# Kernel tuning notes

Measured on AMD Instinct MI355X. Metric: run time of the kernel, lower is better.

## Reference

```python
import jax, jax.numpy as jnp
import numpy as np

N_NODES = 200000
N_EDGES = 1000000
N_GRAPHS = 4096
F_IN = 11
H = 64


def setup_inputs() -> dict:
    key = jax.random.key(0)
    ks = jax.random.split(key, 8)
    x = jax.random.normal(ks[0], (N_NODES, F_IN), jnp.float32)
    edge_index = jax.random.randint(ks[1], (2, N_EDGES), 0, N_NODES, jnp.int32)
    batch = jnp.sort(jax.random.randint(ks[2], (N_NODES,), 0, N_GRAPHS, jnp.int32))
    def glorot(k, shape):
        fan_in, fan_out = shape[0], shape[1]
        s = jnp.sqrt(6.0 / (fan_in + fan_out))
        return jax.random.uniform(k, shape, jnp.float32, -s, s)
    return {
        "x": x,
        "edge_index": edge_index,
        "batch": batch,
        "W1": glorot(ks[3], (F_IN, H)),
        "b1": jnp.zeros((H,), jnp.float32),
        "W2": glorot(ks[4], (H, H)),
        "b2": jnp.zeros((H,), jnp.float32),
        "W3": glorot(ks[5], (H, H)),
        "b3": jnp.zeros((H,), jnp.float32),
        "lin_w": glorot(ks[6], (H, 1)),
        "lin_b": jnp.zeros((1,), jnp.float32),
    }


def _gcn_conv(x, W, b, src, dst, norm, num_nodes):
    # linear transform then gather-scale-scatter (PyG GCNConv, source_to_target)
    h = x @ W                                   # [N, out]
    msg = h[src] * norm[:, None]                # [E+N, out]
    out = jax.ops.segment_sum(msg, dst, num_segments=num_nodes)
    return out + b


def reference(x, edge_index, batch, W1, b1, W2, b2, W3, b3, lin_w, lin_b):
    n = x.shape[0]
    # add self-loops (gcn_norm with add_self_loops=True)
    loops = jnp.arange(n, dtype=edge_index.dtype)
    src = jnp.concatenate([edge_index[0], loops])
    dst = jnp.concatenate([edge_index[1], loops])
    deg = jax.ops.segment_sum(jnp.ones_like(dst, x.dtype), dst, num_segments=n)
    dis = jnp.where(deg > 0, jax.lax.rsqrt(jnp.maximum(deg, 1.0)), 0.0)
    norm = dis[src] * dis[dst]                  # symmetric normalization

    h = jax.nn.relu(_gcn_conv(x, W1, b1, src, dst, norm, n))
    h = jax.nn.relu(_gcn_conv(h, W2, b2, src, dst, norm, n))
    h = _gcn_conv(h, W3, b3, src, dst, norm, n)  # no relu after conv3

    # global mean pool over graph ids
    sums = jax.ops.segment_sum(h, batch, num_segments=N_GRAPHS)
    cnts = jax.ops.segment_sum(jnp.ones((n,), h.dtype), batch, num_segments=N_GRAPHS)
    pooled = sums / jnp.maximum(cnts, 1.0)[:, None]
    # dropout is identity in eval mode
    return pooled @ lin_w + lin_b
```

## Files before the change

kernel.cpp:

```cpp
#include <hip/hip_runtime.h>
#include <hip/hip_fp16.h>

#define N_NODES 200000
#define N_EDGES 1000000
#define N_GRAPHS 4096
#define F_IN 11
#define H 64
#define XP 16
#define CAP 32


__global__ void place_direct_kernel(const int* __restrict__ src, const int* __restrict__ dst,
                                    int* __restrict__ cnt, int* __restrict__ csr) {
    int e = blockIdx.x * blockDim.x + threadIdx.x;
    if (e < N_EDGES) {
        int d = dst[e];
        int p = atomicAdd(&cnt[d], 1);
        if (p < CAP) csr[(size_t)d * CAP + p] = src[e];
    }
}

__global__ void dis_cnt_kernel(const int* __restrict__ cnt, const int* __restrict__ batch,
                               float* __restrict__ dis, int* __restrict__ gcnt) {
    int i = blockIdx.x * blockDim.x + threadIdx.x;
    if (i < N_NODES) {
        dis[i] = rsqrtf((float)(cnt[i] + 1));
        atomicAdd(&gcnt[batch[i]], 1);
    }
}


__global__ void w3l_kernel(const float* __restrict__ W3, const float* __restrict__ lw,
                           float* __restrict__ w3l) {
    int k = threadIdx.x;
    if (k < H) {
        float s = 0.f;
#pragma unroll
        for (int j = 0; j < H; ++j) s += W3[k * H + j] * lw[j];
        w3l[k] = s;
    }
}


__global__ void xscale_kernel(const float* __restrict__ x, const float* __restrict__ dis,
                              __half* __restrict__ xsh) {
    int i = blockIdx.x * blockDim.x + threadIdx.x;
    if (i < N_NODES * XP) {
        int row = i >> 4;
        int c = i & 15;
        float v = (c < F_IN) ? x[(size_t)row * F_IN + c] * dis[row] : 0.f;
        xsh[i] = __float2half_rn(v);
    }
}


__global__ void gather1_kernel(const int* __restrict__ cnt, const int* __restrict__ csr,
                               const __half* __restrict__ xsh, const float* __restrict__ dis,
                               __half* __restrict__ P) {
    int lane = threadIdx.x & 63;
    int j = lane & 3;
    int g = lane >> 2;
    int wave = (blockIdx.x * blockDim.x + threadIdx.x) >> 6;
    int nw = (gridDim.x * blockDim.x) >> 6;
    for (int n = wave; n < N_NODES; n += nw) {
        int deg = cnt[n]; if (deg > CAP) deg = CAP;
        int nslots = deg + 1;
        const int* crow = csr + (size_t)n * CAP;
        __half2 hacc0 = __float2half2_rn(0.f);
        __half2 hacc1 = __float2half2_rn(0.f);
        for (int base = 0; base < nslots; base += 16) {
            int slot = base + g;
            if (slot < nslots) {
                int s = (slot == 0) ? n : crow[slot - 1];
                union { uint2 u; __half2 h[2]; } r;
                r.u = *(const uint2*)(xsh + (size_t)s * XP + j * 4);
                hacc0 = __hadd2(hacc0, r.h[0]);
                hacc1 = __hadd2(hacc1, r.h[1]);
            }
        }
        float2 f0 = __half22float2(hacc0);
        float2 f1 = __half22float2(hacc1);
        float a0 = f0.x, a1 = f0.y, a2 = f1.x, a3 = f1.y;
#pragma unroll
        for (int m = 4; m <= 32; m <<= 1) {
            a0 += __shfl_xor(a0, m, 64);
            a1 += __shfl_xor(a1, m, 64);
            a2 += __shfl_xor(a2, m, 64);
            a3 += __shfl_xor(a3, m, 64);
        }
        if (g == 0) {
            float d = dis[n];
            union { uint2 u; __half2 h[2]; } pk;
            pk.h[0] = __floats2half2_rn(a0 * d, a1 * d);
            pk.h[1] = __floats2half2_rn(a2 * d, a3 * d);
            *(uint2*)(P + (size_t)n * XP + j * 4) = pk.u;
        }
    }
}


__global__ void gemm_fused_kernel(const __half* __restrict__ Ph,
                                  const float* __restrict__ W1, const float* __restrict__ b1,
                                  const float* __restrict__ W2, const float* __restrict__ dis,
                                  __half* __restrict__ Bsh) {
    __shared__ float Xt[XP][68];
    __shared__ float W1s[F_IN][64];
    __shared__ float H1t[64][68];
    __shared__ float W2s[64][64];
    int tid = threadIdx.x;
    int rowbase = blockIdx.x * 64;

    for (int i = tid; i < F_IN * 64; i += 256) W1s[i >> 6][i & 63] = W1[i];
    for (int i = tid; i < 64 * 64; i += 256) W2s[i >> 6][i & 63] = W2[i];
    {
        int r = tid >> 2;
        int c4 = (tid & 3) * 4;
        union { uint2 u; __half2 h[2]; } v;
        v.u = *(const uint2*)(Ph + (size_t)(rowbase + r) * XP + c4);
        float2 f0 = __half22float2(v.h[0]);
        float2 f1 = __half22float2(v.h[1]);
        Xt[c4 + 0][r] = f0.x;
        Xt[c4 + 1][r] = f0.y;
        Xt[c4 + 2][r] = f1.x;
        Xt[c4 + 3][r] = f1.y;
    }
    __syncthreads();

    int tc = (tid & 15) * 4;
    int tr = (tid >> 4) * 4;

    {
        float a[4][4] = {{0}};
#pragma unroll
        for (int k = 0; k < F_IN; ++k) {
            float4 xv = *(const float4*)&Xt[k][tr];
            float4 wv = *(const float4*)&W1s[k][tc];
            float xs4[4] = {xv.x, xv.y, xv.z, xv.w};
            float ws4[4] = {wv.x, wv.y, wv.z, wv.w};
#pragma unroll
            for (int i = 0; i < 4; ++i)
#pragma unroll
                for (int j = 0; j < 4; ++j) a[i][j] += xs4[i] * ws4[j];
        }
        float4 bv = *(const float4*)(b1 + tc);
        float bj[4] = {bv.x, bv.y, bv.z, bv.w};
#pragma unroll
        for (int i = 0; i < 4; ++i)
#pragma unroll
            for (int j = 0; j < 4; ++j)
                H1t[tc + j][tr + i] = fmaxf(a[i][j] + bj[j], 0.f);
    }
    __syncthreads();

    float c00 = 0, c01 = 0, c02 = 0, c03 = 0;
    float c10 = 0, c11 = 0, c12 = 0, c13 = 0;
    float c20 = 0, c21 = 0, c22 = 0, c23 = 0;
    float c30 = 0, c31 = 0, c32 = 0, c33 = 0;
#pragma unroll
    for (int k = 0; k < 64; ++k) {
        float4 xv = *(const float4*)&H1t[k][tr];
        float4 wv = *(const float4*)&W2s[k][tc];
        c00 += xv.x * wv.x; c01 += xv.x * wv.y; c02 += xv.x * wv.z; c03 += xv.x * wv.w;
        c10 += xv.y * wv.x; c11 += xv.y * wv.y; c12 += xv.y * wv.z; c13 += xv.y * wv.w;
        c20 += xv.z * wv.x; c21 += xv.z * wv.y; c22 += xv.z * wv.z; c23 += xv.z * wv.w;
        c30 += xv.w * wv.x; c31 += xv.w * wv.y; c32 += xv.w * wv.z; c33 += xv.w * wv.w;
    }
    float cc[4][4] = {{c00, c01, c02, c03}, {c10, c11, c12, c13},
                      {c20, c21, c22, c23}, {c30, c31, c32, c33}};
#pragma unroll
    for (int i = 0; i < 4; ++i) {
        int row = rowbase + tr + i;
        float d = dis[row];
        union { uint2 u; __half2 h[2]; } pk;
        pk.h[0] = __floats2half2_rn(cc[i][0] * d, cc[i][1] * d);
        pk.h[1] = __floats2half2_rn(cc[i][2] * d, cc[i][3] * d);
        *(uint2*)(Bsh + (size_t)row * 64 + tc) = pk.u;
    }
}


__global__ void gather_fused_kernel(const int* __restrict__ cnt,
                                    const int* __restrict__ csr,
                                    const __half* __restrict__ Bsh,
                                    const float* __restrict__ dis,
                                    const float* __restrict__ b2,
                                    const float* __restrict__ w3l,
                                    float* __restrict__ y) {
    int lane = threadIdx.x & 63;
    int j = lane & 7;
    int g = lane >> 3;
    int wave = (blockIdx.x * blockDim.x + threadIdx.x) >> 6;
    int nw = (gridDim.x * blockDim.x) >> 6;
    float4 bi0 = *(const float4*)(b2 + j * 8);
    float4 bi1 = *(const float4*)(b2 + j * 8 + 4);
    float4 wl0 = *(const float4*)(w3l + j * 8);
    float4 wl1 = *(const float4*)(w3l + j * 8 + 4);
    for (int n = wave; n < N_NODES; n += nw) {
        int deg = cnt[n]; if (deg > CAP) deg = CAP;
        int nslots = deg + 1;
        const int* crow = csr + (size_t)n * CAP;
        __half2 hacc[4];
#pragma unroll
        for (int k = 0; k < 4; ++k) hacc[k] = __float2half2_rn(0.f);
        for (int base = 0; base < nslots; base += 8) {
            int slot = base + g;
            if (slot < nslots) {
                int s = (slot == 0) ? n : crow[slot - 1];
                union { uint4 u; __half2 h[4]; } r;
                r.u = *(const uint4*)(Bsh + (size_t)s * 64 + j * 8);
#pragma unroll
                for (int k = 0; k < 4; ++k) hacc[k] = __hadd2(hacc[k], r.h[k]);
            }
        }
        float acc[8];
#pragma unroll
        for (int k = 0; k < 4; ++k) {
            float2 f = __half22float2(hacc[k]);
            acc[2 * k] = f.x; acc[2 * k + 1] = f.y;
        }
#pragma unroll
        for (int m = 8; m <= 32; m <<= 1) {
#pragma unroll
            for (int k = 0; k < 8; ++k) acc[k] += __shfl_xor(acc[k], m, 64);
        }
        if (g == 0) {
            float d = dis[n];
            float bi[8] = {bi0.x, bi0.y, bi0.z, bi0.w, bi1.x, bi1.y, bi1.z, bi1.w};
            float wl[8] = {wl0.x, wl0.y, wl0.z, wl0.w, wl1.x, wl1.y, wl1.z, wl1.w};
            float p = 0.f;
#pragma unroll
            for (int k = 0; k < 8; ++k)
                p += fmaxf(acc[k] * d + bi[k], 0.f) * wl[k];
            p += __shfl_xor(p, 1, 64);
            p += __shfl_xor(p, 2, 64);
            p += __shfl_xor(p, 4, 64);
            if (j == 0) y[n] = p * d;
        }
    }
}


__global__ void pool_scalar_kernel(const int* __restrict__ cnt,
                                   const int* __restrict__ csr,
                                   const float* __restrict__ y,
                                   const float* __restrict__ dis,
                                   const int* __restrict__ batch,
                                   float* __restrict__ gsum) {
    int lane = threadIdx.x & 63;
    int u = lane >> 4;
    int t = lane & 15;
    int wave = (blockIdx.x * blockDim.x + threadIdx.x) >> 6;
    int n = wave * 4 + u;
    int deg = cnt[n]; if (deg > CAP) deg = CAP;
    int nslots = deg + 1;
    const int* crow = csr + (size_t)n * CAP;
    float acc = 0.f;
    for (int base = 0; base < nslots; base += 16) {
        int slot = base + t;
        if (slot < nslots) {
            int s = (slot == 0) ? n : crow[slot - 1];
            acc += y[s];
        }
    }
    acc += __shfl_xor(acc, 1, 64);
    acc += __shfl_xor(acc, 2, 64);
    acc += __shfl_xor(acc, 4, 64);
    acc += __shfl_xor(acc, 8, 64);
    if (t == 0) atomicAdd(&gsum[batch[n]], acc * dis[n]);
}


__global__ void head2_kernel(const float* __restrict__ gsum, const int* __restrict__ gcnt,
                             const float* __restrict__ b3, const float* __restrict__ lw,
                             const float* __restrict__ lb, float* __restrict__ out) {
    int g = blockIdx.x * blockDim.x + threadIdx.x;
    if (g >= N_GRAPHS) return;
    float cb = 0.f;
#pragma unroll
    for (int k = 0; k < H; ++k) cb += b3[k] * lw[k];
    int c = gcnt[g];
    out[g] = (c > 0) ? (gsum[g] / (float)c + cb + lb[0]) : lb[0];
}

extern "C" void kernel_launch(void* const* d_in, const int* in_sizes, int n_in,
                              void* d_out, int out_size, void* d_ws, size_t ws_size,
                              hipStream_t stream) {
    const float* x     = (const float*)d_in[0];
    const int*   ei    = (const int*)d_in[1];
    const int*   batch = (const int*)d_in[2];
    const float* W1    = (const float*)d_in[3];
    const float* b1    = (const float*)d_in[4];
    const float* W2    = (const float*)d_in[5];
    const float* b2    = (const float*)d_in[6];
    const float* W3    = (const float*)d_in[7];
    const float* b3    = (const float*)d_in[8];
    const float* lw    = (const float*)d_in[9];
    const float* lb    = (const float*)d_in[10];
    float* out = (float*)d_out;

    const int* src = ei;
    const int* dst = ei + N_EDGES;

    char* ws = (char*)d_ws;
    const size_t MB = 1u << 20;
    int*    cnt  = (int*)ws;
    float*  y    = (float*)(ws + 1 * MB);
    float*  dis  = (float*)(ws + 2 * MB);
    int*    csr  = (int*)(ws + 4 * MB);
    __half* xsh  = (__half*)(ws + 30 * MB);
    __half* Ph   = (__half*)(ws + 37 * MB);
    __half* Bsh  = (__half*)(ws + 44 * MB);
    float*  gsum = (float*)(ws + 70 * MB);
    int*    gcnt = (int*)(ws + 70 * MB + 16384);
    float*  w3l  = (float*)(ws + 70 * MB + 32768);

    const int BT = 256;
    const int gemm_grid = N_NODES / 64;
    const int gath_grid = 2048;

    hipMemsetAsync(cnt, 0, (size_t)N_NODES * 4, stream);
    hipMemsetAsync(gsum, 0, (size_t)N_GRAPHS * 8, stream);
    place_direct_kernel<<<(N_EDGES + BT - 1) / BT, BT, 0, stream>>>(src, dst, cnt, csr);
    dis_cnt_kernel<<<(N_NODES + BT - 1) / BT, BT, 0, stream>>>(cnt, batch, dis, gcnt);
    w3l_kernel<<<1, 64, 0, stream>>>(W3, lw, w3l);

    xscale_kernel<<<(N_NODES * XP + BT - 1) / BT, BT, 0, stream>>>(x, dis, xsh);
    gather1_kernel<<<gath_grid, BT, 0, stream>>>(cnt, csr, xsh, dis, Ph);
    gemm_fused_kernel<<<gemm_grid, BT, 0, stream>>>(Ph, W1, b1, W2, dis, Bsh);

    gather_fused_kernel<<<gath_grid, BT, 0, stream>>>(cnt, csr, Bsh, dis, b2, w3l, y);

    pool_scalar_kernel<<<N_NODES / 16, BT, 0, stream>>>(cnt, csr, y, dis, batch, gsum);

    head2_kernel<<<(N_GRAPHS + BT - 1) / BT, BT, 0, stream>>>(gsum, gcnt, b3, lw, lb, out);
}
```

Baseline: 394.2 us.

## Fuse degree normalization into xscale, process two nodes per wave in gathers

Removes the separate dis_cnt kernel by computing rsqrt degree and the per-graph node counts inside xscale_kernel. Both gather kernels now handle two nodes per wave iteration, interleaving their neighbor loads for more memory-level parallelism at the cost of extra registers and divergence when degrees differ. The pooling kernel uses 8 lanes per node instead of 16, covering more nodes per wave. Each lane recomputes rsqrt from cnt, which adds redundant loads.

```diff
diff --git a/kernel.cpp b/kernel.cpp
--- a/kernel.cpp
+++ b/kernel.cpp
@@ -20,15 +20,6 @@
     }
 }
 
-__global__ void dis_cnt_kernel(const int* __restrict__ cnt, const int* __restrict__ batch,
-                               float* __restrict__ dis, int* __restrict__ gcnt) {
-    int i = blockIdx.x * blockDim.x + threadIdx.x;
-    if (i < N_NODES) {
-        dis[i] = rsqrtf((float)(cnt[i] + 1));
-        atomicAdd(&gcnt[batch[i]], 1);
-    }
-}
-
 
 __global__ void w3l_kernel(const float* __restrict__ W3, const float* __restrict__ lw,
                            float* __restrict__ w3l) {
@@ -42,13 +33,19 @@
 }
 
 
-__global__ void xscale_kernel(const float* __restrict__ x, const float* __restrict__ dis,
-                              __half* __restrict__ xsh) {
+__global__ void xscale_kernel(const float* __restrict__ x, const int* __restrict__ cnt,
+                              const int* __restrict__ batch, float* __restrict__ dis,
+                              int* __restrict__ gcnt, __half* __restrict__ xsh) {
     int i = blockIdx.x * blockDim.x + threadIdx.x;
     if (i < N_NODES * XP) {
         int row = i >> 4;
         int c = i & 15;
-        float v = (c < F_IN) ? x[(size_t)row * F_IN + c] * dis[row] : 0.f;
+        float d = rsqrtf((float)(cnt[row] + 1));
+        if (c == 0) {
+            dis[row] = d;
+            atomicAdd(&gcnt[batch[row]], 1);
+        }
+        float v = (c < F_IN) ? x[(size_t)row * F_IN + c] * d : 0.f;
         xsh[i] = __float2half_rn(v);
     }
 }
@@ -62,38 +59,54 @@
     int g = lane >> 2;
     int wave = (blockIdx.x * blockDim.x + threadIdx.x) >> 6;
     int nw = (gridDim.x * blockDim.x) >> 6;
-    for (int n = wave; n < N_NODES; n += nw) {
-        int deg = cnt[n]; if (deg > CAP) deg = CAP;
-        int nslots = deg + 1;
-        const int* crow = csr + (size_t)n * CAP;
-        __half2 hacc0 = __float2half2_rn(0.f);
-        __half2 hacc1 = __float2half2_rn(0.f);
-        for (int base = 0; base < nslots; base += 16) {
+    for (int n0 = wave * 2; n0 < N_NODES; n0 += nw * 2) {
+        int n1 = n0 + 1;
+        int d0 = cnt[n0]; if (d0 > CAP) d0 = CAP;
+        int d1 = cnt[n1]; if (d1 > CAP) d1 = CAP;
+        int ns0 = d0 + 1, ns1 = d1 + 1;
+        const int* crow0 = csr + (size_t)n0 * CAP;
+        const int* crow1 = csr + (size_t)n1 * CAP;
+        __half2 a0h0 = __float2half2_rn(0.f), a0h1 = a0h0;
+        __half2 a1h0 = a0h0, a1h1 = a0h0;
+        int maxns = ns0 > ns1 ? ns0 : ns1;
+        for (int base = 0; base < maxns; base += 16) {
             int slot = base + g;
-            if (slot < nslots) {
-                int s = (slot == 0) ? n : crow[slot - 1];
+            if (slot < ns0) {
+                int s = (slot == 0) ? n0 : crow0[slot - 1];
                 union { uint2 u; __half2 h[2]; } r;
                 r.u = *(const uint2*)(xsh + (size_t)s * XP + j * 4);
-                hacc0 = __hadd2(hacc0, r.h[0]);
-                hacc1 = __hadd2(hacc1, r.h[1]);
-            }
-        }
-        float2 f0 = __half22float2(hacc0);
-        float2 f1 = __half22float2(hacc1);
-        float a0 = f0.x, a1 = f0.y, a2 = f1.x, a3 = f1.y;
+                a0h0 = __hadd2(a0h0, r.h[0]);
+                a0h1 = __hadd2(a0h1, r.h[1]);
+            }
+            if (slot < ns1) {
+                int s = (slot == 0) ? n1 : crow1[slot - 1];
+                union { uint2 u; __half2 h[2]; } r;
+                r.u = *(const uint2*)(xsh + (size_t)s * XP + j * 4);
+                a1h0 = __hadd2(a1h0, r.h[0]);
+                a1h1 = __hadd2(a1h1, r.h[1]);
+            }
+        }
+        float2 f00 = __half22float2(a0h0), f01 = __half22float2(a0h1);
+        float2 f10 = __half22float2(a1h0), f11 = __half22float2(a1h1);
+        float v0[4] = {f00.x, f00.y, f01.x, f01.y};
+        float v1[4] = {f10.x, f10.y, f11.x, f11.y};
 #pragma unroll
         for (int m = 4; m <= 32; m <<= 1) {
-            a0 += __shfl_xor(a0, m, 64);
-            a1 += __shfl_xor(a1, m, 64);
-            a2 += __shfl_xor(a2, m, 64);
-            a3 += __shfl_xor(a3, m, 64);
+#pragma unroll
+            for (int k = 0; k < 4; ++k) {
+                v0[k] += __shfl_xor(v0[k], m, 64);
+                v1[k] += __shfl_xor(v1[k], m, 64);
+            }
         }
         if (g == 0) {
-            float d = dis[n];
+            float dd0 = dis[n0], dd1 = dis[n1];
             union { uint2 u; __half2 h[2]; } pk;
-            pk.h[0] = __floats2half2_rn(a0 * d, a1 * d);
-            pk.h[1] = __floats2half2_rn(a2 * d, a3 * d);
-            *(uint2*)(P + (size_t)n * XP + j * 4) = pk.u;
+            pk.h[0] = __floats2half2_rn(v0[0] * dd0, v0[1] * dd0);
+            pk.h[1] = __floats2half2_rn(v0[2] * dd0, v0[3] * dd0);
+            *(uint2*)(P + (size_t)n0 * XP + j * 4) = pk.u;
+            pk.h[0] = __floats2half2_rn(v1[0] * dd1, v1[1] * dd1);
+            pk.h[1] = __floats2half2_rn(v1[2] * dd1, v1[3] * dd1);
+            *(uint2*)(P + (size_t)n1 * XP + j * 4) = pk.u;
         }
     }
 }
@@ -195,46 +208,69 @@
     float4 bi1 = *(const float4*)(b2 + j * 8 + 4);
     float4 wl0 = *(const float4*)(w3l + j * 8);
     float4 wl1 = *(const float4*)(w3l + j * 8 + 4);
-    for (int n = wave; n < N_NODES; n += nw) {
-        int deg = cnt[n]; if (deg > CAP) deg = CAP;
-        int nslots = deg + 1;
-        const int* crow = csr + (size_t)n * CAP;
-        __half2 hacc[4];
-#pragma unroll
-        for (int k = 0; k < 4; ++k) hacc[k] = __float2half2_rn(0.f);
-        for (int base = 0; base < nslots; base += 8) {
+    for (int n0 = wave * 2; n0 < N_NODES; n0 += nw * 2) {
+        int n1 = n0 + 1;
+        int d0 = cnt[n0]; if (d0 > CAP) d0 = CAP;
+        int d1 = cnt[n1]; if (d1 > CAP) d1 = CAP;
+        int ns0 = d0 + 1, ns1 = d1 + 1;
+        const int* crow0 = csr + (size_t)n0 * CAP;
+        const int* crow1 = csr + (size_t)n1 * CAP;
+        __half2 ha[4], hb[4];
+#pragma unroll
+        for (int k = 0; k < 4; ++k) { ha[k] = __float2half2_rn(0.f); hb[k] = ha[k]; }
+        int maxns = ns0 > ns1 ? ns0 : ns1;
+        for (int base = 0; base < maxns; base += 8) {
             int slot = base + g;
-            if (slot < nslots) {
-                int s = (slot == 0) ? n : crow[slot - 1];
+            if (slot < ns0) {
+                int s = (slot == 0) ? n0 : crow0[slot - 1];
                 union { uint4 u; __half2 h[4]; } r;
                 r.u = *(const uint4*)(Bsh + (size_t)s * 64 + j * 8);
 #pragma unroll
-                for (int k = 0; k < 4; ++k) hacc[k] = __hadd2(hacc[k], r.h[k]);
-            }
-        }
-        float acc[8];
+                for (int k = 0; k < 4; ++k) ha[k] = __hadd2(ha[k], r.h[k]);
+            }
+            if (slot < ns1) {
+                int s = (slot == 0) ? n1 : crow1[slot - 1];
+                union { uint4 u; __half2 h[4]; } r;
+                r.u = *(const uint4*)(Bsh + (size_t)s * 64 + j * 8);
+#pragma unroll
+                for (int k = 0; k < 4; ++k) hb[k] = __hadd2(hb[k], r.h[k]);
+            }
+        }
+        float acc0[8], acc1[8];
 #pragma unroll
         for (int k = 0; k < 4; ++k) {
-            float2 f = __half22float2(hacc[k]);
-            acc[2 * k] = f.x; acc[2 * k + 1] = f.y;
+            float2 f = __half22float2(ha[k]);
+            acc0[2 * k] = f.x; acc0[2 * k + 1] = f.y;
+            f = __half22float2(hb[k]);
+            acc1[2 * k] = f.x; acc1[2 * k + 1] = f.y;
         }
 #pragma unroll
         for (int m = 8; m <= 32; m <<= 1) {
 #pragma unroll
-            for (int k = 0; k < 8; ++k) acc[k] += __shfl_xor(acc[k], m, 64);
+            for (int k = 0; k < 8; ++k) {
+                acc0[k] += __shfl_xor(acc0[k], m, 64);
+                acc1[k] += __shfl_xor(acc1[k], m, 64);
+            }
         }
         if (g == 0) {
-            float d = dis[n];
             float bi[8] = {bi0.x, bi0.y, bi0.z, bi0.w, bi1.x, bi1.y, bi1.z, bi1.w};
             float wl[8] = {wl0.x, wl0.y, wl0.z, wl0.w, wl1.x, wl1.y, wl1.z, wl1.w};
-            float p = 0.f;
-#pragma unroll
-            for (int k = 0; k < 8; ++k)
-                p += fmaxf(acc[k] * d + bi[k], 0.f) * wl[k];
-            p += __shfl_xor(p, 1, 64);
-            p += __shfl_xor(p, 2, 64);
-            p += __shfl_xor(p, 4, 64);
-            if (j == 0) y[n] = p * d;
+            float dd0 = dis[n0], dd1 = dis[n1];
+            float p0 = 0.f, p1 = 0.f;
+#pragma unroll
+            for (int k = 0; k < 8; ++k) {
+                p0 += fmaxf(acc0[k] * dd0 + bi[k], 0.f) * wl[k];
+                p1 += fmaxf(acc1[k] * dd1 + bi[k], 0.f) * wl[k];
+            }
+#pragma unroll
+            for (int m = 1; m <= 4; m <<= 1) {
+                p0 += __shfl_xor(p0, m, 64);
+                p1 += __shfl_xor(p1, m, 64);
+            }
+            if (j == 0) {
+                y[n0] = p0 * dd0;
+                y[n1] = p1 * dd1;
+            }
         }
     }
 }
@@ -247,15 +283,15 @@
                                    const int* __restrict__ batch,
                                    float* __restrict__ gsum) {
     int lane = threadIdx.x & 63;
-    int u = lane >> 4;
-    int t = lane & 15;
+    int u = lane >> 3;
+    int t = lane & 7;
     int wave = (blockIdx.x * blockDim.x + threadIdx.x) >> 6;
-    int n = wave * 4 + u;
+    int n = wave * 8 + u;
     int deg = cnt[n]; if (deg > CAP) deg = CAP;
     int nslots = deg + 1;
     const int* crow = csr + (size_t)n * CAP;
     float acc = 0.f;
-    for (int base = 0; base < nslots; base += 16) {
+    for (int base = 0; base < nslots; base += 8) {
         int slot = base + t;
         if (slot < nslots) {
             int s = (slot == 0) ? n : crow[slot - 1];
@@ -265,7 +301,6 @@
     acc += __shfl_xor(acc, 1, 64);
     acc += __shfl_xor(acc, 2, 64);
     acc += __shfl_xor(acc, 4, 64);
-    acc += __shfl_xor(acc, 8, 64);
     if (t == 0) atomicAdd(&gsum[batch[n]], acc * dis[n]);
 }
 
@@ -321,16 +356,16 @@
     hipMemsetAsync(cnt, 0, (size_t)N_NODES * 4, stream);
     hipMemsetAsync(gsum, 0, (size_t)N_GRAPHS * 8, stream);
     place_direct_kernel<<<(N_EDGES + BT - 1) / BT, BT, 0, stream>>>(src, dst, cnt, csr);
-    dis_cnt_kernel<<<(N_NODES + BT - 1) / BT, BT, 0, stream>>>(cnt, batch, dis, gcnt);
     w3l_kernel<<<1, 64, 0, stream>>>(W3, lw, w3l);
 
-    xscale_kernel<<<(N_NODES * XP + BT - 1) / BT, BT, 0, stream>>>(x, dis, xsh);
+    xscale_kernel<<<(N_NODES * XP + BT - 1) / BT, BT, 0, stream>>>(x, cnt, batch, dis,
+                                                                   gcnt, xsh);
     gather1_kernel<<<gath_grid, BT, 0, stream>>>(cnt, csr, xsh, dis, Ph);
     gemm_fused_kernel<<<gemm_grid, BT, 0, stream>>>(Ph, W1, b1, W2, dis, Bsh);
 
     gather_fused_kernel<<<gath_grid, BT, 0, stream>>>(cnt, csr, Bsh, dis, b2, w3l, y);
 
-    pool_scalar_kernel<<<N_NODES / 16, BT, 0, stream>>>(cnt, csr, y, dis, batch, gsum);
+    pool_scalar_kernel<<<N_NODES / 32, BT, 0, stream>>>(cnt, csr, y, dis, batch, gsum);
 
     head2_kernel<<<(N_GRAPHS + BT - 1) / BT, BT, 0, stream>>>(gsum, gcnt, b3, lw, lb, out);
 }
```

Result: slower. 412.1 us (+4.6%).
